# Optimization experiments

Hardware: AMD Instinct MI355X
Metric: run time of the kernel (lower is better)

The kernel has to match this reference:

```python
import jax, jax.numpy as jnp
import numpy as np

B, T, C, H = 2, 2048, 1024, 16
N = C // H
TM_DIM, TD_DIM = 32, 64
EPS = 1e-5 * 8 ** 2  # GroupNorm eps from the module


def setup_inputs() -> dict:
    key = jax.random.key(0)
    ks = jax.random.split(key, 16)
    nrm = lambda k, shp, s: jax.random.normal(k, shp, dtype=jnp.float32) * s
    uni = lambda k, shp, a: jax.random.uniform(k, shp, jnp.float32, -a, a)
    ddd = (jnp.arange(C, dtype=jnp.float32) / C).reshape(1, 1, C)
    return {
        "x": nrm(ks[0], (B, T, C), 1.0),
        "time_maa_x": 1.0 - ddd ** 0.5,
        "time_maa_w": 1.0 - ddd ** 0.5,
        "time_maa_k": 1.0 - ddd ** 0.5,
        "time_maa_v": 1.0 - (ddd ** 0.5 + 0.15),
        "time_maa_r": 1.0 - ddd ** 0.25,
        "time_maa_g": 1.0 - ddd ** 0.25,
        "time_maa_w1": uni(ks[1], (C, 5 * TM_DIM), 1e-4),
        "time_maa_w2": uni(ks[2], (5, TM_DIM, C), 1e-4),
        "time_decay": jnp.linspace(-6.0, -1.0, C).astype(jnp.float32).reshape(1, 1, C),
        "time_decay_w1": uni(ks[3], (C, TD_DIM), 1e-4),
        "time_decay_w2": uni(ks[4], (TD_DIM, C), 1e-4),
        "time_faaaa": nrm(ks[5], (H, N), 0.1),
        "W_r": nrm(ks[6], (C, C), C ** -0.5),
        "W_k": nrm(ks[7], (C, C), C ** -0.5),
        "W_v": nrm(ks[8], (C, C), C ** -0.5),
        "W_g": nrm(ks[9], (C, C), C ** -0.5),
        "W_o": nrm(ks[10], (C, C), C ** -0.5),
        "ln_w": jnp.ones((C,), jnp.float32),
        "ln_b": jnp.zeros((C,), jnp.float32),
    }


def _forward(x, tmx, tmw, tmk, tmv, tmr, tmg, maa_w1, maa_w2, tdecay, td_w1,
             td_w2, u, Wr, Wk, Wv, Wg, Wo, ln_w, ln_b):
    Bq, Tq, Cq = x.shape
    # time_shift: x[t-1] with zero at t=0
    xx = jnp.concatenate([jnp.zeros_like(x[:, :1]), x[:, :-1]], axis=1) - x
    xxx = x + xx * tmx
    t5 = jnp.tanh(xxx @ maa_w1).reshape(Bq, Tq, 5, TM_DIM)
    m = jnp.einsum('btfe,fec->fbtc', t5, maa_w2)  # [5,B,T,C] data-dependent mix
    xw = x + xx * (tmw + m[0])
    xk = x + xx * (tmk + m[1])
    xv = x + xx * (tmv + m[2])
    xr = x + xx * (tmr + m[3])
    xg = x + xx * (tmg + m[4])
    r = xr @ Wr
    k = xk @ Wk
    v = xv @ Wv
    g = jax.nn.silu(xg @ Wg)
    w = tdecay + jnp.tanh(xw @ td_w1) @ td_w2          # [B,T,C] log-log decay
    decay = jnp.exp(-jnp.exp(w))                        # in (0,1)
    to_tbhn = lambda a: a.reshape(Bq, Tq, H, N).transpose(1, 0, 2, 3)
    rT, kT, vT, dT = (to_tbhn(a) for a in (r, k, v, decay))

    def step(S, inp):  # S: [B,H,N,N] (key_dim i, value_dim j)
        r_t, k_t, v_t, d_t = inp
        kv = k_t[..., :, None] * v_t[..., None, :]
        y = jnp.einsum('bhi,bhij->bhj', r_t, S + u[None, :, :, None] * kv)
        return d_t[..., None] * S + kv, y

    S0 = jnp.zeros((Bq, H, N, N), x.dtype)
    _, ys = jax.lax.scan(step, S0, (rT, kT, vT, dT))
    y = ys.transpose(1, 0, 2, 3).reshape(Bq, Tq, Cq)
    # GroupNorm with H groups over channels
    yh = y.reshape(Bq, Tq, H, N)
    mu = yh.mean(-1, keepdims=True)
    var = yh.var(-1, keepdims=True)
    yn = (yh - mu) / jnp.sqrt(var + EPS)
    yn = (yn * ln_w.reshape(H, N) + ln_b.reshape(H, N)).reshape(Bq, Tq, Cq)
    return (yn * g) @ Wo


def reference(x, time_maa_x, time_maa_w, time_maa_k, time_maa_v, time_maa_r,
              time_maa_g, time_maa_w1, time_maa_w2, time_decay, time_decay_w1,
              time_decay_w2, time_faaaa, W_r, W_k, W_v, W_g, W_o, ln_w, ln_b):
    return _forward(x, time_maa_x, time_maa_w, time_maa_k, time_maa_v,
                    time_maa_r, time_maa_g, time_maa_w1, time_maa_w2,
                    time_decay, time_decay_w1, time_decay_w2, time_faaaa,
                    W_r, W_k, W_v, W_g, W_o, ln_w, ln_b)
```

## Files before the change

### kernel.cpp

```cpp
#include <hip/hip_runtime.h>
#include <hip/hip_bf16.h>
#include <cstdint>
#include <cstddef>

#define B_ 2
#define T_ 2048
#define C_ 1024
#define H_ 16
#define NCH 32
#define CHL 64

typedef unsigned short ushort_t;
typedef __bf16 bf16x8 __attribute__((ext_vector_type(8)));
typedef float f32x4 __attribute__((ext_vector_type(4)));

__device__ __forceinline__ ushort_t f2bf(float f) {
  union { float f; uint32_t u; } x; x.f = f;
  uint32_t r = x.u + 0x7fffu + ((x.u >> 16) & 1u);
  return (ushort_t)(r >> 16);
}
__device__ __forceinline__ float bf2f(ushort_t h) {
  union { uint32_t u; float f; } x; x.u = (uint32_t)h << 16; return x.f;
}

__device__ __forceinline__ void gload16(const void* g, void* l) {
  __builtin_amdgcn_global_load_lds(
      (const __attribute__((address_space(1))) void*)g,
      (__attribute__((address_space(3))) void*)l, 16, 0, 0);
}

#define FENCE() asm volatile("" ::: "memory")
#define BAR() do { FENCE(); __builtin_amdgcn_s_barrier(); FENCE(); } while (0)

__device__ __forceinline__ void stb(ushort_t* tile, int row, int col, ushort_t v) {
  *(ushort_t*)((char*)tile + row * 128 + ((col * 2) ^ ((row & 7) << 4))) = v;
}
__device__ __forceinline__ bf16x8 ldb(const ushort_t* tile, int row, int kbyte) {
  return *(const bf16x8*)((const char*)tile + row * 128 + (kbyte ^ ((row & 7) << 4)));
}

struct TDesc { const float* src; ushort_t* dst; int R, Cc, Cpad; };
struct TArgs { TDesc d[9]; };

__global__ __launch_bounds__(256) void transpose_cvt(TArgs args) {
  TDesc D = args.d[blockIdx.z];
  int c0 = blockIdx.x * 32, r0 = blockIdx.y * 32;
  if (c0 >= D.Cpad || r0 >= D.R) return;
  __shared__ float tile[32][33];
  int tx = threadIdx.x & 31, ty = threadIdx.x >> 5;
#pragma unroll
  for (int i = 0; i < 32; i += 8) {
    int r = r0 + ty + i, c = c0 + tx;
    tile[ty + i][tx] = (r < D.R && c < D.Cc) ? D.src[(size_t)r * D.Cc + c] : 0.f;
  }
  __syncthreads();
#pragma unroll
  for (int i = 0; i < 32; i += 8) {
    int c = c0 + ty + i, r = r0 + tx;
    if (c < D.Cpad && r < D.R) D.dst[(size_t)c * D.R + r] = f2bf(tile[tx][ty + i]);
  }
}

__global__ __launch_bounds__(256) void prep_kernel(
    const float* __restrict__ x, const float* __restrict__ tmx,
    float* __restrict__ xx, ushort_t* __restrict__ xxx) {
  size_t idx = ((size_t)blockIdx.x * 256 + threadIdx.x) * 4;
  int tt = (int)((idx >> 10) & (T_ - 1));
  int c = (int)(idx & (C_ - 1));
  float4 xv = *(const float4*)&x[idx];
  float4 xp;
  if (tt == 0) { xp.x = xp.y = xp.z = xp.w = 0.f; }
  else xp = *(const float4*)&x[idx - C_];
  float4 tm = *(const float4*)&tmx[c];
  float4 d;
  d.x = xp.x - xv.x; d.y = xp.y - xv.y; d.z = xp.z - xv.z; d.w = xp.w - xv.w;
  *(float4*)&xx[idx] = d;
  xxx[idx + 0] = f2bf(xv.x + d.x * tm.x);
  xxx[idx + 1] = f2bf(xv.y + d.y * tm.y);
  xxx[idx + 2] = f2bf(xv.z + d.z * tm.z);
  xxx[idx + 3] = f2bf(xv.w + d.w * tm.w);
}

template <int EPI>
__global__ __launch_bounds__(256) void gemm_bt(
    const ushort_t* __restrict__ A, int lda,
    const ushort_t* __restrict__ Bt, int ldb,
    void* __restrict__ Cp, int ldc, int K,
    const float* __restrict__ aux2) {
  __shared__ ushort_t sA[128 * 32];
  __shared__ ushort_t sB[128 * 32];
  const int t = threadIdx.x;
  const int l = t & 63;
  const int w = t >> 6;
  const int wm = w >> 1, wn = w & 1;
  const int m0 = blockIdx.x * 128, n0 = blockIdx.y * 128;
  const int lr = l & 15;
  const int lk = (l >> 4) * 8;

  f32x4 acc[4][4] = {};

  for (int kt = 0; kt < K; kt += 32) {
    __syncthreads();
#pragma unroll
    for (int it = 0; it < 2; ++it) {
      int cbase = it * 256 + w * 64;
      int ca = cbase + l;
      int row = ca >> 2, kc = ca & 3;
      gload16(A + (size_t)(m0 + row) * lda + kt + kc * 8, (char*)sA + (size_t)cbase * 16);
      gload16(Bt + (size_t)(n0 + row) * ldb + kt + kc * 8, (char*)sB + (size_t)cbase * 16);
    }
    __syncthreads();
    bf16x8 af[4], bfr[4];
#pragma unroll
    for (int mi = 0; mi < 4; ++mi)
      af[mi] = *(const bf16x8*)&sA[(wm * 64 + mi * 16 + lr) * 32 + lk];
#pragma unroll
    for (int ni = 0; ni < 4; ++ni)
      bfr[ni] = *(const bf16x8*)&sB[(wn * 64 + ni * 16 + lr) * 32 + lk];
#pragma unroll
    for (int mi = 0; mi < 4; ++mi)
#pragma unroll
      for (int ni = 0; ni < 4; ++ni)
        acc[mi][ni] = __builtin_amdgcn_mfma_f32_16x16x32_bf16(af[mi], bfr[ni], acc[mi][ni], 0, 0, 0);
  }
#pragma unroll
  for (int mi = 0; mi < 4; ++mi) {
#pragma unroll
    for (int ni = 0; ni < 4; ++ni) {
      int col = n0 + wn * 64 + ni * 16 + lr;
#pragma unroll
      for (int r = 0; r < 4; ++r) {
        int row = m0 + wm * 64 + mi * 16 + (l >> 4) * 4 + r;
        float v = acc[mi][ni][r];
        size_t idx = (size_t)row * ldc + col;
        if constexpr (EPI == 0) {
          ((float*)Cp)[idx] = v;
        } else if constexpr (EPI == 4) {
          ((float*)Cp)[idx] = __expf(aux2[col] + v);
        }
      }
    }
  }
}

__global__ __launch_bounds__(256) void gemm_bt64(
    const ushort_t* __restrict__ A, int lda,
    const ushort_t* __restrict__ Bt, int ldb,
    ushort_t* __restrict__ Cp, int ldc, int K) {
  __shared__ ushort_t sA[64 * 32];
  __shared__ ushort_t sB[128 * 32];
  const int t = threadIdx.x;
  const int l = t & 63;
  const int w = t >> 6;
  const int m0 = blockIdx.x * 64, n0 = blockIdx.y * 128;
  const int lr = l & 15, lk = (l >> 4) * 8;

  f32x4 acc[4][2] = {};
  for (int kt = 0; kt < K; kt += 32) {
    __syncthreads();
    {
      int row = t >> 2, kc = t & 3;
      gload16(A + (size_t)(m0 + row) * lda + kt + kc * 8, (char*)sA + w * 1024);
    }
#pragma unroll
    for (int it = 0; it < 2; ++it) {
      int ca = it * 256 + t;
      int row = ca >> 2, kc = ca & 3;
      gload16(Bt + (size_t)(n0 + row) * ldb + kt + kc * 8,
              (char*)sB + it * 4096 + w * 1024);
    }
    __syncthreads();
    bf16x8 af[4], bfr[2];
#pragma unroll
    for (int mi = 0; mi < 4; ++mi)
      af[mi] = *(const bf16x8*)&sA[(mi * 16 + lr) * 32 + lk];
#pragma unroll
    for (int ni = 0; ni < 2; ++ni)
      bfr[ni] = *(const bf16x8*)&sB[(w * 32 + ni * 16 + lr) * 32 + lk];
#pragma unroll
    for (int mi = 0; mi < 4; ++mi)
#pragma unroll
      for (int ni = 0; ni < 2; ++ni)
        acc[mi][ni] = __builtin_amdgcn_mfma_f32_16x16x32_bf16(af[mi], bfr[ni], acc[mi][ni], 0, 0, 0);
  }
#pragma unroll
  for (int mi = 0; mi < 4; ++mi)
#pragma unroll
    for (int ni = 0; ni < 2; ++ni) {
      int col = n0 + w * 32 + ni * 16 + lr;
#pragma unroll
      for (int r = 0; r < 4; ++r) {
        int row = m0 + mi * 16 + (l >> 4) * 4 + r;
        Cp[(size_t)row * ldc + col] = f2bf(tanhf(acc[mi][ni][r]));
      }
    }
}

struct PDesc { const ushort_t* A; const ushort_t* Bt; float* C; int epi; };
struct PArgs { PDesc d[4]; };

__global__ __launch_bounds__(512, 1) void gemm_proj256(PArgs args) {
  PDesc D = args.d[blockIdx.z];
  __shared__ ushort_t sA[2][16384], sB[2][16384];
  const int tid = threadIdx.x;
  const int w = tid >> 6, l = tid & 63;
  const int wm = w >> 2, wn = w & 3;
  const int lr = l & 15, hi4 = l >> 4;
  const int m0 = blockIdx.x * 256, n0 = blockIdx.y * 256;

  const int srow = tid >> 3;
  const int acol = (((tid & 7) ^ (srow & 7)) << 3);
  const ushort_t* Ag = D.A + (size_t)(m0 + srow) * C_ + acol;
  const ushort_t* Bg = D.Bt + (size_t)(n0 + srow) * C_ + acol;
  const int dst16 = tid * 16;

  f32x4 acc[8][4] = {};

#define STAGE(b, kt)                                                   \
  do {                                                                 \
    gload16(Ag + (kt),            (char*)sA[b] + 0 * 8192 + dst16);    \
    gload16(Ag + (kt) +  64 * C_, (char*)sA[b] + 1 * 8192 + dst16);    \
    gload16(Ag + (kt) + 128 * C_, (char*)sA[b] + 2 * 8192 + dst16);    \
    gload16(Ag + (kt) + 192 * C_, (char*)sA[b] + 3 * 8192 + dst16);    \
    gload16(Bg + (kt),            (char*)sB[b] + 0 * 8192 + dst16);    \
    gload16(Bg + (kt) +  64 * C_, (char*)sB[b] + 1 * 8192 + dst16);    \
    gload16(Bg + (kt) + 128 * C_, (char*)sB[b] + 2 * 8192 + dst16);    \
    gload16(Bg + (kt) + 192 * C_, (char*)sB[b] + 3 * 8192 + dst16);    \
  } while (0)

#define LA(b, kk, mi)                                                        \
  (*(const bf16x8*)((const char*)sA[b] + (wm * 128 + (mi)*16 + lr) * 128 +   \
                    ((((kk)*4 + hi4) ^ (lr & 7)) << 4)))
#define LB(b, kk, ni)                                                        \
  (*(const bf16x8*)((const char*)sB[b] + (wn * 64 + (ni)*16 + lr) * 128 +    \
                    ((((kk)*4 + hi4) ^ (lr & 7)) << 4)))

#define COMP(b)                                                              \
  do {                                                                       \
    __builtin_amdgcn_s_setprio(1);                                           \
    _Pragma("unroll")                                                        \
    for (int kk = 0; kk < 2; ++kk) {                                         \
      bf16x8 bfr[4];                                                         \
      _Pragma("unroll")                                                      \
      for (int ni = 0; ni < 4; ++ni) bfr[ni] = LB(b, kk, ni);                \
      _Pragma("unroll")                                                      \
      for (int mi = 0; mi < 8; ++mi) {                                       \
        bf16x8 af = LA(b, kk, mi);                                           \
        _Pragma("unroll")                                                    \
        for (int ni = 0; ni < 4; ++ni)                                       \
          acc[mi][ni] = __builtin_amdgcn_mfma_f32_16x16x32_bf16(             \
              af, bfr[ni], acc[mi][ni], 0, 0, 0);                            \
      }                                                                      \
    }                                                                        \
    __builtin_amdgcn_s_setprio(0);                                           \
  } while (0)

#define BODY(b, jj)                                                          \
  do {                                                                       \
    COMP(b);                                                                 \
    BAR();                                                                   \
    if ((jj) < 14) {                                                         \
      STAGE(b, ((jj) + 2) * 64);                                             \
      asm volatile("s_waitcnt vmcnt(8)" ::: "memory");                       \
    } else if ((jj) == 14) {                                                 \
      asm volatile("s_waitcnt vmcnt(0)" ::: "memory");                       \
    }                                                                        \
    BAR();                                                                   \
  } while (0)

  STAGE(0, 0);
  STAGE(1, 64);
  asm volatile("s_waitcnt vmcnt(8)" ::: "memory");
  BAR();

#pragma unroll 1
  for (int j = 0; j < 16; j += 2) {
    BODY(0, j);
    BODY(1, j + 1);
  }

  const int epi = D.epi;
#pragma unroll
  for (int mi = 0; mi < 8; ++mi)
#pragma unroll
    for (int ni = 0; ni < 4; ++ni) {
      int col = n0 + wn * 64 + ni * 16 + lr;
#pragma unroll
      for (int r = 0; r < 4; ++r) {
        int row = m0 + wm * 128 + mi * 16 + hi4 * 4 + r;
        float v = acc[mi][ni][r];
        if (epi) v = v / (1.f + __expf(-v));
        D.C[(size_t)row * C_ + col] = v;
      }
    }
#undef BODY
#undef COMP
#undef LB
#undef LA
#undef STAGE
}

struct MixArgs { const float* tm[5]; ushort_t* dst[5]; };

__global__ __launch_bounds__(256) void fused_mix(
    const float* __restrict__ x, const float* __restrict__ xx,
    const ushort_t* __restrict__ t5, const ushort_t* __restrict__ w2t,
    MixArgs margs) {
  __shared__ float xs[64 * 128];
  __shared__ float xxs[64 * 128];
  __shared__ ushort_t sA[64 * 32];
  __shared__ ushort_t sB[128 * 32];
  const int t = threadIdx.x;
  const int l = t & 63;
  const int w = t >> 6;
  const int wm = w >> 1, wn = w & 1;
  const int m0 = blockIdx.x * 64, n0 = blockIdx.y * 128;
  const int lr = l & 15;
  const int lk = (l >> 4) * 8;

#pragma unroll
  for (int it = 0; it < 8; ++it) {
    int row = it * 8 + (t >> 5);
    int c16 = t & 31;
    gload16(x + (size_t)(m0 + row) * C_ + n0 + c16 * 4, (char*)xs + row * 512 + c16 * 16);
    gload16(xx + (size_t)(m0 + row) * C_ + n0 + c16 * 4, (char*)xxs + row * 512 + c16 * 16);
  }

  for (int f = 0; f < 5; ++f) {
    __syncthreads();
    {
      int row = t >> 2, c8 = t & 3;
      gload16(t5 + (size_t)(m0 + row) * 256 + f * 32 + c8 * 8, (char*)sA + t * 16);
    }
#pragma unroll
    for (int it = 0; it < 2; ++it) {
      int row = it * 64 + (t >> 2), c8 = t & 3;
      gload16(w2t + (size_t)(n0 + row) * 160 + f * 32 + c8 * 8,
              (char*)sB + it * 4096 + t * 16);
    }
    __syncthreads();
    bf16x8 af[2], bfr[4];
#pragma unroll
    for (int mi = 0; mi < 2; ++mi)
      af[mi] = *(const bf16x8*)&sA[(wm * 32 + mi * 16 + lr) * 32 + lk];
#pragma unroll
    for (int ni = 0; ni < 4; ++ni)
      bfr[ni] = *(const bf16x8*)&sB[(wn * 64 + ni * 16 + lr) * 32 + lk];
    f32x4 acc[2][4] = {};
#pragma unroll
    for (int mi = 0; mi < 2; ++mi)
#pragma unroll
      for (int ni = 0; ni < 4; ++ni)
        acc[mi][ni] = __builtin_amdgcn_mfma_f32_16x16x32_bf16(af[mi], bfr[ni], acc[mi][ni], 0, 0, 0);
    const float* tmf = margs.tm[f];
    ushort_t* dst = margs.dst[f];
#pragma unroll
    for (int mi = 0; mi < 2; ++mi) {
#pragma unroll
      for (int ni = 0; ni < 4; ++ni) {
        int cl = wn * 64 + ni * 16 + lr;
        int col = n0 + cl;
        float tmv = tmf[col];
#pragma unroll
        for (int r = 0; r < 4; ++r) {
          int rl = wm * 32 + mi * 16 + (l >> 4) * 4 + r;
          int row = m0 + rl;
          float xv = xs[rl * 128 + cl];
          float xxv = xxs[rl * 128 + cl];
          dst[(size_t)row * C_ + col] = f2bf(xv + xxv * (tmv + acc[mi][ni][r]));
        }
      }
    }
  }
}

__global__ __launch_bounds__(256) void chunk_local(
    const float* __restrict__ rx, const float* __restrict__ kx,
    const float* __restrict__ vx, const float* __restrict__ lamx,
    const float* __restrict__ u, float* __restrict__ Mt,
    float* __restrict__ aLg, ushort_t* __restrict__ rAg,
    float* __restrict__ yo) {
  int c = blockIdx.x, bh = blockIdx.y;
  int b = bh >> 4, h = bh & 15;
  __shared__ ushort_t sRA[64 * 64], sKA[64 * 64], sKh[64 * 64], sKl[64 * 64],
                      sVh[64 * 64], sVl[64 * 64], sP[64 * 64];
  __shared__ float qsum[4][64];
  __shared__ float ruk[64];
  const int tid = threadIdx.x;
  const int i = tid & 63;
  const int q = tid >> 6;
  size_t base = ((size_t)b * T_ + (size_t)c * CHL) * C_ + h * 64;
  size_t cb = ((size_t)c * 32 + bh);

  float lam[16];
  float run = 0.f;
#pragma unroll
  for (int s = 0; s < 16; ++s) {
    lam[s] = lamx[base + (size_t)(q * 16 + s) * C_ + i];
    run += lam[s];
  }
  qsum[q][i] = run;
  __syncthreads();
  float pre = 0.f, ct = 0.f;
#pragma unroll
  for (int qq = 0; qq < 4; ++qq) {
    float vq = qsum[qq][i];
    ct += vq;
    if (qq < q) pre += vq;
  }
  float uu = u[h * 64 + i];
  float ci = pre;
#pragma unroll
  for (int s = 0; s < 16; ++s) {
    int t = q * 16 + s;
    ci += lam[s];
    float cl = ci - lam[s];
    size_t o = base + (size_t)t * C_ + i;
    float rv = rx[o], kv = kx[o], vv = vx[o];
    ushort_t ra = f2bf(rv * __expf(-cl));
    stb(sRA, t, i, ra);
    rAg[cb * 4096 + t * 64 + i] = ra;
    stb(sKA, t, i, f2bf(kv * __expf(ci)));
    float kal = kv * __expf(ci - ct);
    ushort_t khv = f2bf(kal);
    stb(sKh, i, t, khv);
    stb(sKl, i, t, f2bf(kal - bf2f(khv)));
    ushort_t vhv = f2bf(vv);
    stb(sVh, i, t, vhv);
    stb(sVl, i, t, f2bf(vv - bf2f(vhv)));
    float rr = rv * uu * kv;
#pragma unroll
    for (int m = 32; m; m >>= 1) rr += __shfl_xor(rr, m);
    if (i == 0) ruk[t] = rr;
  }
  if (q == 0) aLg[cb * 64 + i] = __expf(-ct);
  __syncthreads();

  const int l = tid & 63, w = tid >> 6;
  const int wm = w >> 1, wn = w & 1;
  const int lr = l & 15, hi4 = l >> 4;

  {
    f32x4 accP[2][2] = {};
#pragma unroll
    for (int kk = 0; kk < 2; ++kk) {
      bf16x8 af[2], bf_[2];
#pragma unroll
      for (int mi = 0; mi < 2; ++mi) af[mi] = ldb(sRA, wm * 32 + mi * 16 + lr, kk * 64 + hi4 * 16);
#pragma unroll
      for (int ni = 0; ni < 2; ++ni) bf_[ni] = ldb(sKA, wn * 32 + ni * 16 + lr, kk * 64 + hi4 * 16);
#pragma unroll
      for (int mi = 0; mi < 2; ++mi)
#pragma unroll
        for (int ni = 0; ni < 2; ++ni)
          accP[mi][ni] = __builtin_amdgcn_mfma_f32_16x16x32_bf16(af[mi], bf_[ni], accP[mi][ni], 0, 0, 0);
    }
#pragma unroll
    for (int mi = 0; mi < 2; ++mi)
#pragma unroll
      for (int ni = 0; ni < 2; ++ni)
#pragma unroll
        for (int r = 0; r < 4; ++r) {
          int tl = wm * 32 + mi * 16 + hi4 * 4 + r, sl = wn * 32 + ni * 16 + lr;
          float v = accP[mi][ni][r];
          v = sl < tl ? v : (sl == tl ? ruk[tl] : 0.f);
          stb(sP, tl, sl, f2bf(v));
        }
  }
  __syncthreads();

  f32x4 accY[2][2] = {}, accM[2][2] = {};
#pragma unroll
  for (int kk = 0; kk < 2; ++kk) {
    bf16x8 pa[2], vhA[2], vlA[2], vhB[2], vlB[2], khB[2], klB[2];
#pragma unroll
    for (int mi = 0; mi < 2; ++mi) {
      int rw = wm * 32 + mi * 16 + lr;
      pa[mi] = ldb(sP, rw, kk * 64 + hi4 * 16);
      vhA[mi] = ldb(sVh, rw, kk * 64 + hi4 * 16);
      vlA[mi] = ldb(sVl, rw, kk * 64 + hi4 * 16);
    }
#pragma unroll
    for (int ni = 0; ni < 2; ++ni) {
      int rw = wn * 32 + ni * 16 + lr;
      vhB[ni] = ldb(sVh, rw, kk * 64 + hi4 * 16);
      vlB[ni] = ldb(sVl, rw, kk * 64 + hi4 * 16);
      khB[ni] = ldb(sKh, rw, kk * 64 + hi4 * 16);
      klB[ni] = ldb(sKl, rw, kk * 64 + hi4 * 16);
    }
#pragma unroll
    for (int mi = 0; mi < 2; ++mi)
#pragma unroll
      for (int ni = 0; ni < 2; ++ni) {
        accY[mi][ni] = __builtin_amdgcn_mfma_f32_16x16x32_bf16(pa[mi], vhB[ni], accY[mi][ni], 0, 0, 0);
        accY[mi][ni] = __builtin_amdgcn_mfma_f32_16x16x32_bf16(pa[mi], vlB[ni], accY[mi][ni], 0, 0, 0);
        accM[mi][ni] = __builtin_amdgcn_mfma_f32_16x16x32_bf16(vhA[mi], khB[ni], accM[mi][ni], 0, 0, 0);
        accM[mi][ni] = __builtin_amdgcn_mfma_f32_16x16x32_bf16(vhA[mi], klB[ni], accM[mi][ni], 0, 0, 0);
        accM[mi][ni] = __builtin_amdgcn_mfma_f32_16x16x32_bf16(vlA[mi], khB[ni], accM[mi][ni], 0, 0, 0);
      }
  }
#pragma unroll
  for (int mi = 0; mi < 2; ++mi)
#pragma unroll
    for (int ni = 0; ni < 2; ++ni)
#pragma unroll
      for (int r = 0; r < 4; ++r) {
        int rw = wm * 32 + mi * 16 + hi4 * 4 + r;
        int cw = wn * 32 + ni * 16 + lr;
        yo[base + (size_t)rw * C_ + cw] = accY[mi][ni][r];
        Mt[cb * 4096 + rw * 64 + cw] = accM[mi][ni][r];
      }
}

__global__ __launch_bounds__(256) void combine2(
    const float* __restrict__ Mt, const float* __restrict__ aLg,
    ushort_t* __restrict__ S0h, ushort_t* __restrict__ S0l) {
  int bh = blockIdx.x >> 2;
  int ij = ((blockIdx.x & 3) * 256 + threadIdx.x) * 4;
  int i = ij & 63;
  float4 s = {0.f, 0.f, 0.f, 0.f};
  for (int c = 0; c < NCH; ++c) {
    size_t o = ((size_t)c * 32 + bh) * 4096 + ij;
    float4 m = *(const float4*)&Mt[o];
    float4 p = *(const float4*)&aLg[((size_t)c * 32 + bh) * 64 + i];
    ushort4 hi, lo;
    hi.x = f2bf(s.x); lo.x = f2bf(s.x - bf2f(hi.x));
    hi.y = f2bf(s.y); lo.y = f2bf(s.y - bf2f(hi.y));
    hi.z = f2bf(s.z); lo.z = f2bf(s.z - bf2f(hi.z));
    hi.w = f2bf(s.w); lo.w = f2bf(s.w - bf2f(hi.w));
    *(ushort4*)&S0h[o] = hi;
    *(ushort4*)&S0l[o] = lo;
    s.x = p.x * s.x + m.x; s.y = p.y * s.y + m.y;
    s.z = p.z * s.z + m.z; s.w = p.w * s.w + m.w;
  }
}

__global__ __launch_bounds__(256) void inter_gn(
    const ushort_t* __restrict__ rAg, const ushort_t* __restrict__ S0h,
    const ushort_t* __restrict__ S0l, const float* __restrict__ yin,
    const float* __restrict__ gx, const float* __restrict__ lnw,
    const float* __restrict__ lnb, ushort_t* __restrict__ Z) {
  int c = blockIdx.x, bh = blockIdx.y;
  int b = bh >> 4, h = bh & 15;
  __shared__ ushort_t sRA[64 * 64], sSh[64 * 64], sSl[64 * 64];
  __shared__ float st[64][2][2];
  const int tid = threadIdx.x;
  size_t cb = ((size_t)c * 32 + bh) * 4096;
#pragma unroll
  for (int it = 0; it < 2; ++it) {
    int lb = tid * 32 + it * 16;
    int row = lb >> 7, wi = lb & 127;
    int so = row * 128 + (wi ^ ((row & 7) << 4));
    *(uint4*)((char*)sRA + so) = *(const uint4*)((const char*)(rAg + cb) + lb);
    *(uint4*)((char*)sSh + so) = *(const uint4*)((const char*)(S0h + cb) + lb);
    *(uint4*)((char*)sSl + so) = *(const uint4*)((const char*)(S0l + cb) + lb);
  }
  const int l = tid & 63, w = tid >> 6;
  const int wm = w >> 1, wn = w & 1;
  const int lr = l & 15, hi4 = l >> 4;
  size_t base = ((size_t)b * T_ + (size_t)c * CHL) * C_ + h * 64;

  f32x4 acc[2][2];
#pragma unroll
  for (int mi = 0; mi < 2; ++mi)
#pragma unroll
    for (int ni = 0; ni < 2; ++ni)
#pragma unroll
      for (int r = 0; r < 4; ++r)
        acc[mi][ni][r] = yin[base + (size_t)(wm * 32 + mi * 16 + hi4 * 4 + r) * C_ +
                             wn * 32 + ni * 16 + lr];
  __syncthreads();
#pragma unroll
  for (int kk = 0; kk < 2; ++kk) {
    bf16x8 af[2], bh_[2], bl_[2];
#pragma unroll
    for (int mi = 0; mi < 2; ++mi) af[mi] = ldb(sRA, wm * 32 + mi * 16 + lr, kk * 64 + hi4 * 16);
#pragma unroll
    for (int ni = 0; ni < 2; ++ni) {
      bh_[ni] = ldb(sSh, wn * 32 + ni * 16 + lr, kk * 64 + hi4 * 16);
      bl_[ni] = ldb(sSl, wn * 32 + ni * 16 + lr, kk * 64 + hi4 * 16);
    }
#pragma unroll
    for (int mi = 0; mi < 2; ++mi)
#pragma unroll
      for (int ni = 0; ni < 2; ++ni) {
        acc[mi][ni] = __builtin_amdgcn_mfma_f32_16x16x32_bf16(af[mi], bh_[ni], acc[mi][ni], 0, 0, 0);
        acc[mi][ni] = __builtin_amdgcn_mfma_f32_16x16x32_bf16(af[mi], bl_[ni], acc[mi][ni], 0, 0, 0);
      }
  }
#pragma unroll
  for (int mi = 0; mi < 2; ++mi)
#pragma unroll
    for (int r = 0; r < 4; ++r) {
      int row = wm * 32 + mi * 16 + hi4 * 4 + r;
      float s1 = acc[mi][0][r] + acc[mi][1][r];
      float s2 = acc[mi][0][r] * acc[mi][0][r] + acc[mi][1][r] * acc[mi][1][r];
#pragma unroll
      for (int m = 1; m < 16; m <<= 1) { s1 += __shfl_xor(s1, m); s2 += __shfl_xor(s2, m); }
      if (lr == 0) { st[row][wn][0] = s1; st[row][wn][1] = s2; }
    }
  __syncthreads();
#pragma unroll
  for (int mi = 0; mi < 2; ++mi)
#pragma unroll
    for (int ni = 0; ni < 2; ++ni)
#pragma unroll
      for (int r = 0; r < 4; ++r) {
        int row = wm * 32 + mi * 16 + hi4 * 4 + r;
        int jl = wn * 32 + ni * 16 + lr;
        float S1 = st[row][0][0] + st[row][1][0];
        float S2 = st[row][0][1] + st[row][1][1];
        float mu = S1 * (1.f / 64.f);
        float var = S2 * (1.f / 64.f) - mu * mu;
        float rs = rsqrtf(var + 6.4e-4f);
        int col = h * 64 + jl;
        size_t o = base + (size_t)row * C_ + jl;
        float yn = (acc[mi][ni][r] - mu) * rs * lnw[col] + lnb[col];
        Z[o] = f2bf(yn * gx[o]);
      }
}

extern "C" void kernel_launch(void* const* d_in, const int* in_sizes, int n_in,
                              void* d_out, int out_size, void* d_ws, size_t ws_size,
                              hipStream_t stream) {
  const float* x    = (const float*)d_in[0];
  const float* tmx  = (const float*)d_in[1];
  const float* tmw  = (const float*)d_in[2];
  const float* tmk  = (const float*)d_in[3];
  const float* tmv  = (const float*)d_in[4];
  const float* tmr  = (const float*)d_in[5];
  const float* tmg  = (const float*)d_in[6];
  const float* maaw1 = (const float*)d_in[7];
  const float* maaw2 = (const float*)d_in[8];
  const float* tdec = (const float*)d_in[9];
  const float* tdw1 = (const float*)d_in[10];
  const float* tdw2 = (const float*)d_in[11];
  const float* u    = (const float*)d_in[12];
  const float* Wr   = (const float*)d_in[13];
  const float* Wk   = (const float*)d_in[14];
  const float* Wv   = (const float*)d_in[15];
  const float* Wg   = (const float*)d_in[16];
  const float* Wo   = (const float*)d_in[17];
  const float* lnw  = (const float*)d_in[18];
  const float* lnb  = (const float*)d_in[19];

  char* ws = (char*)d_ws;
  const size_t MB = 1ull << 20;
  float*    xx     = (float*)(ws + 0);
  ushort_t* xxx    = (ushort_t*)(ws + 16 * MB);
  ushort_t* WrT    = (ushort_t*)(ws + 24 * MB);
  ushort_t* WkT    = (ushort_t*)(ws + 26 * MB);
  ushort_t* WvT    = (ushort_t*)(ws + 28 * MB);
  ushort_t* WgT    = (ushort_t*)(ws + 30 * MB);
  ushort_t* WoT    = (ushort_t*)(ws + 32 * MB);
  ushort_t* maaW1T = (ushort_t*)(ws + 34 * MB);
  ushort_t* tdW1T  = (ushort_t*)(ws + 35 * MB);
  ushort_t* tdW2T  = (ushort_t*)(ws + 35 * MB + 256 * 1024);
  ushort_t* maaW2T = (ushort_t*)(ws + 35 * MB + 512 * 1024);
  ushort_t* t5     = (ushort_t*)(ws + 36 * MB);
  ushort_t* t5d    = (ushort_t*)(ws + 38 * MB);
  ushort_t* Xm[5];
  for (int f = 0; f < 5; ++f) Xm[f] = (ushort_t*)(ws + 40 * MB + (size_t)f * 8 * MB);
  float*    Mtb = (float*)(ws + 40 * MB);
  ushort_t* S0h = (ushort_t*)(ws + 56 * MB);
  ushort_t* S0l = (ushort_t*)(ws + 64 * MB);
  ushort_t* rAg = (ushort_t*)(ws + 72 * MB);
  float* rb   = (float*)(ws + 80 * MB);
  float* kb   = (float*)(ws + 96 * MB);
  float* vb   = (float*)(ws + 112 * MB);
  float* gb   = (float*)(ws + 128 * MB);
  float* lam  = (float*)(ws + 144 * MB);
  float* aLg  = (float*)(ws + 160 * MB);
  float* yb   = (float*)(ws + 0);
  ushort_t* Zb = (ushort_t*)(ws + 16 * MB);

  TArgs ta;
  ta.d[0] = TDesc{Wr,    WrT,    1024, 1024, 1024};
  ta.d[1] = TDesc{Wk,    WkT,    1024, 1024, 1024};
  ta.d[2] = TDesc{Wv,    WvT,    1024, 1024, 1024};
  ta.d[3] = TDesc{Wg,    WgT,    1024, 1024, 1024};
  ta.d[4] = TDesc{Wo,    WoT,    1024, 1024, 1024};
  ta.d[5] = TDesc{maaw1, maaW1T, 1024, 160,  256};
  ta.d[6] = TDesc{tdw1,  tdW1T,  1024, 64,   128};
  ta.d[7] = TDesc{tdw2,  tdW2T,  64,   1024, 1024};
  ta.d[8] = TDesc{maaw2, maaW2T, 160,  1024, 1024};
  transpose_cvt<<<dim3(32, 32, 9), 256, 0, stream>>>(ta);

  prep_kernel<<<(B_ * T_ * C_) / 1024, 256, 0, stream>>>(x, tmx, xx, xxx);

  gemm_bt64<<<dim3(64, 2), 256, 0, stream>>>(xxx, C_, maaW1T, C_, t5, 256, C_);

  MixArgs ma;
  ma.tm[0] = tmw; ma.tm[1] = tmk; ma.tm[2] = tmv; ma.tm[3] = tmr; ma.tm[4] = tmg;
  for (int f = 0; f < 5; ++f) ma.dst[f] = Xm[f];
  fused_mix<<<dim3(64, 8), 256, 0, stream>>>(x, xx, t5, maaW2T, ma);

  PArgs pa;
  pa.d[0] = PDesc{Xm[3], WrT, rb, 0};
  pa.d[1] = PDesc{Xm[1], WkT, kb, 0};
  pa.d[2] = PDesc{Xm[2], WvT, vb, 0};
  pa.d[3] = PDesc{Xm[4], WgT, gb, 1};
  gemm_proj256<<<dim3(16, 4, 4), 512, 0, stream>>>(pa);

  gemm_bt64<<<dim3(64, 1), 256, 0, stream>>>(Xm[0], C_, tdW1T, C_, t5d, 128, C_);
  gemm_bt<4><<<dim3(32, 8), 256, 0, stream>>>(t5d, 128, tdW2T, 64, lam, C_, 64, tdec);

  chunk_local<<<dim3(NCH, B_ * H_), 256, 0, stream>>>(rb, kb, vb, lam, u, Mtb, aLg, rAg, yb);
  combine2<<<128, 256, 0, stream>>>(Mtb, aLg, S0h, S0l);
  inter_gn<<<dim3(NCH, B_ * H_), 256, 0, stream>>>(rAg, S0h, S0l, yb, gb, lnw, lnb, Zb);

  gemm_bt<0><<<dim3(32, 8), 256, 0, stream>>>(Zb, C_, WoT, C_, (float*)d_out, C_, C_, nullptr);
}
```

Before: 214.2 us.

## Restructure 256x256 projection GEMM into 4-phase interleaved load/compute pipeline

Splits each K-tile of the projection GEMM into four phases. Each phase loads a slice of A fragments from LDS, issues a pair of global-to-LDS prefetch loads for quarter-tiles of later K steps, then runs a block of MFMAs. This spreads memory traffic across the compute instead of issuing all prefetches between full tiles, aiming to hide latency better. It adds more barriers per tile and extra prefetch loads that wrap around the K range past the final iteration, which cost redundant bandwidth.

Result: no change. 210.4 us (-1.8%).

```diff
diff --git a/kernel.cpp b/kernel.cpp
--- a/kernel.cpp
+++ b/kernel.cpp
@@ -201,7 +201,7 @@
 
 __global__ __launch_bounds__(512, 1) void gemm_proj256(PArgs args) {
   PDesc D = args.d[blockIdx.z];
-  __shared__ ushort_t sA[2][16384], sB[2][16384];
+  __shared__ ushort_t sMem[2][2][4][4096];
   const int tid = threadIdx.x;
   const int w = tid >> 6, l = tid & 63;
   const int wm = w >> 2, wn = w & 3;
@@ -209,75 +209,85 @@
   const int m0 = blockIdx.x * 256, n0 = blockIdx.y * 256;
 
   const int srow = tid >> 3;
-  const int acol = (((tid & 7) ^ (srow & 7)) << 3);
-  const ushort_t* Ag = D.A + (size_t)(m0 + srow) * C_ + acol;
-  const ushort_t* Bg = D.Bt + (size_t)(n0 + srow) * C_ + acol;
+  const int scol = (((tid & 7) ^ (srow & 7)) << 3);
+  const ushort_t* Abase = D.A + (size_t)(m0 + srow) * C_ + scol;
+  const ushort_t* Bbase = D.Bt + (size_t)(n0 + srow) * C_ + scol;
   const int dst16 = tid * 16;
 
   f32x4 acc[8][4] = {};
-
-#define STAGE(b, kt)                                                   \
-  do {                                                                 \
-    gload16(Ag + (kt),            (char*)sA[b] + 0 * 8192 + dst16);    \
-    gload16(Ag + (kt) +  64 * C_, (char*)sA[b] + 1 * 8192 + dst16);    \
-    gload16(Ag + (kt) + 128 * C_, (char*)sA[b] + 2 * 8192 + dst16);    \
-    gload16(Ag + (kt) + 192 * C_, (char*)sA[b] + 3 * 8192 + dst16);    \
-    gload16(Bg + (kt),            (char*)sB[b] + 0 * 8192 + dst16);    \
-    gload16(Bg + (kt) +  64 * C_, (char*)sB[b] + 1 * 8192 + dst16);    \
-    gload16(Bg + (kt) + 128 * C_, (char*)sB[b] + 2 * 8192 + dst16);    \
-    gload16(Bg + (kt) + 192 * C_, (char*)sB[b] + 3 * 8192 + dst16);    \
+  bf16x8 bfr[2][4];
+
+#define STG_A(db, unit, kt) \
+  gload16(Abase + (size_t)(unit) * 64 * C_ + (kt), (char*)&sMem[db][0][unit][0] + dst16)
+#define STG_B(db, unit, kt) \
+  gload16(Bbase + (size_t)(unit) * 64 * C_ + (kt), (char*)&sMem[db][1][unit][0] + dst16)
+
+#define LDA_(b, p, i, kk)                                                      \
+  (*(const bf16x8*)((const char*)&sMem[b][0][wm * 2 + ((p) >> 1)][0] +         \
+                    (((2 * (p) + (i)) & 3) * 16 + lr) * 128 +                  \
+                    ((((kk)*4 + hi4) ^ (lr & 7)) << 4)))
+#define LDB_(b, ni, kk)                                                        \
+  (*(const bf16x8*)((const char*)&sMem[b][1][wn][0] +                          \
+                    ((ni)*16 + lr) * 128 + ((((kk)*4 + hi4) ^ (lr & 7)) << 4)))
+
+#define PH(b, p, STAGES, VM)                                                   \
+  do {                                                                         \
+    bf16x8 a00, a10, a01, a11;                                                 \
+    if ((p) == 0) {                                                            \
+      _Pragma("unroll") for (int kk = 0; kk < 2; ++kk)                         \
+      _Pragma("unroll") for (int ni = 0; ni < 4; ++ni)                         \
+        bfr[kk][ni] = LDB_(b, ni, kk);                                         \
+    }                                                                          \
+    a00 = LDA_(b, p, 0, 0); a10 = LDA_(b, p, 1, 0);                            \
+    a01 = LDA_(b, p, 0, 1); a11 = LDA_(b, p, 1, 1);                            \
+    STAGES;                                                                    \
+    VM;                                                                        \
+    BAR();                                                                     \
+    asm volatile("s_waitcnt lgkmcnt(0)" ::: "memory");                         \
+    __builtin_amdgcn_sched_barrier(0);                                         \
+    __builtin_amdgcn_s_setprio(1);                                             \
+    _Pragma("unroll") for (int ni = 0; ni < 4; ++ni) {                         \
+      acc[2 * (p)][ni] = __builtin_amdgcn_mfma_f32_16x16x32_bf16(              \
+          a00, bfr[0][ni], acc[2 * (p)][ni], 0, 0, 0);                         \
+      acc[2 * (p) + 1][ni] = __builtin_amdgcn_mfma_f32_16x16x32_bf16(          \
+          a10, bfr[0][ni], acc[2 * (p) + 1][ni], 0, 0, 0);                     \
+      acc[2 * (p)][ni] = __builtin_amdgcn_mfma_f32_16x16x32_bf16(              \
+          a01, bfr[1][ni], acc[2 * (p)][ni], 0, 0, 0);                         \
+      acc[2 * (p) + 1][ni] = __builtin_amdgcn_mfma_f32_16x16x32_bf16(          \
+          a11, bfr[1][ni], acc[2 * (p) + 1][ni], 0, 0, 0);                     \
+    }                                                                          \
+    __builtin_amdgcn_s_setprio(0);                                             \
+    BAR();                                                                     \
   } while (0)
 
-#define LA(b, kk, mi)                                                        \
-  (*(const bf16x8*)((const char*)sA[b] + (wm * 128 + (mi)*16 + lr) * 128 +   \
-                    ((((kk)*4 + hi4) ^ (lr & 7)) << 4)))
-#define LB(b, kk, ni)                                                        \
-  (*(const bf16x8*)((const char*)sB[b] + (wn * 64 + (ni)*16 + lr) * 128 +    \
-                    ((((kk)*4 + hi4) ^ (lr & 7)) << 4)))
-
-#define COMP(b)                                                              \
-  do {                                                                       \
-    __builtin_amdgcn_s_setprio(1);                                           \
-    _Pragma("unroll")                                                        \
-    for (int kk = 0; kk < 2; ++kk) {                                         \
-      bf16x8 bfr[4];                                                         \
-      _Pragma("unroll")                                                      \
-      for (int ni = 0; ni < 4; ++ni) bfr[ni] = LB(b, kk, ni);                \
-      _Pragma("unroll")                                                      \
-      for (int mi = 0; mi < 8; ++mi) {                                       \
-        bf16x8 af = LA(b, kk, mi);                                           \
-        _Pragma("unroll")                                                    \
-        for (int ni = 0; ni < 4; ++ni)                                       \
-          acc[mi][ni] = __builtin_amdgcn_mfma_f32_16x16x32_bf16(             \
-              af, bfr[ni], acc[mi][ni], 0, 0, 0);                            \
-      }                                                                      \
-    }                                                                        \
-    __builtin_amdgcn_s_setprio(0);                                           \
+#define TILE(b, kt1, kt2)                                                      \
+  do {                                                                         \
+    PH(b, 0, { STG_A((b) ^ 1, 1, kt1); STG_A((b) ^ 1, 3, kt1); }, );           \
+    PH(b, 1, { STG_B(b, 0, kt2); STG_B(b, 1, kt2); },                          \
+       asm volatile("s_waitcnt vmcnt(10)" ::: "memory"));                      \
+    PH(b, 2, { STG_B(b, 2, kt2); STG_B(b, 3, kt2); }, );                       \
+    PH(b, 3, { STG_A(b, 0, kt2); STG_A(b, 2, kt2); },                          \
+       asm volatile("s_waitcnt vmcnt(8)" ::: "memory"));                       \
   } while (0)
 
-#define BODY(b, jj)                                                          \
-  do {                                                                       \
-    COMP(b);                                                                 \
-    BAR();                                                                   \
-    if ((jj) < 14) {                                                         \
-      STAGE(b, ((jj) + 2) * 64);                                             \
-      asm volatile("s_waitcnt vmcnt(8)" ::: "memory");                       \
-    } else if ((jj) == 14) {                                                 \
-      asm volatile("s_waitcnt vmcnt(0)" ::: "memory");                       \
-    }                                                                        \
-    BAR();                                                                   \
-  } while (0)
-
-  STAGE(0, 0);
-  STAGE(1, 64);
+  STG_B(0, 0, 0);  STG_B(0, 1, 0);
+  STG_B(0, 2, 0);  STG_B(0, 3, 0);
+  STG_A(0, 0, 0);  STG_A(0, 2, 0);
+  STG_A(0, 1, 0);  STG_A(0, 3, 0);
+  STG_B(1, 0, 64); STG_B(1, 1, 64);
+  STG_B(1, 2, 64); STG_B(1, 3, 64);
+  STG_A(1, 0, 64); STG_A(1, 2, 64);
   asm volatile("s_waitcnt vmcnt(8)" ::: "memory");
   BAR();
 
 #pragma unroll 1
   for (int j = 0; j < 16; j += 2) {
-    BODY(0, j);
-    BODY(1, j + 1);
-  }
+    int ka1 = ((j + 1) & 15) * 64, ka2 = ((j + 2) & 15) * 64;
+    int kb1 = ((j + 2) & 15) * 64, kb2 = ((j + 3) & 15) * 64;
+    TILE(0, ka1, ka2);
+    TILE(1, kb1, kb2);
+  }
+  asm volatile("s_waitcnt vmcnt(0)" ::: "memory");
 
   const int epi = D.epi;
 #pragma unroll
@@ -293,11 +303,12 @@
         D.C[(size_t)row * C_ + col] = v;
       }
     }
-#undef BODY
-#undef COMP
-#undef LB
-#undef LA
-#undef STAGE
+#undef TILE
+#undef PH
+#undef LDB_
+#undef LDA_
+#undef STG_B
+#undef STG_A
 }
 
 struct MixArgs { const float* tm[5]; ushort_t* dst[5]; };
```
